# Kernel optimization log

Hardware: AMD Instinct MI355X
Metric: run time of the kernel (lower is better)

Reference implementation:

```python
import jax, jax.numpy as jnp
import numpy as np

N, E, G, H, IN = 200000, 400000, 64, 128, 5
LN_EPS = 1e-5


def setup_inputs() -> dict:
    key = jax.random.key(0)
    ks = jax.random.split(key, 32)
    d = {}
    d["x"] = jax.random.normal(ks[0], (N, IN), jnp.float32)
    d["edge_index"] = jax.random.randint(ks[1], (2, E), 0, N, dtype=jnp.int32)
    d["edge_attr"] = jax.random.normal(ks[2], (E, 1), jnp.float32)
    d["batch"] = jnp.sort(jax.random.randint(ks[3], (N,), 0, G, dtype=jnp.int32))
    dims = [IN, H, H]
    i = 4
    names = [("ew", "eb", "w1_", "b1_", "w2_", "b2_", "g", "bt")]
    for l, din in enumerate(dims):
        d[f"ew{l}"] = jax.random.normal(ks[i], (1, din), jnp.float32); i += 1
        d[f"eb{l}"] = jnp.zeros((din,), jnp.float32)
        d[f"w1_{l}"] = jax.random.normal(ks[i], (din, H), jnp.float32) / np.sqrt(din); i += 1
        d[f"b1_{l}"] = jnp.zeros((H,), jnp.float32)
        d[f"w2_{l}"] = jax.random.normal(ks[i], (H, H), jnp.float32) / np.sqrt(H); i += 1
        d[f"b2_{l}"] = jnp.zeros((H,), jnp.float32)
        d[f"g{l}"] = jnp.ones((H,), jnp.float32)
        d[f"bt{l}"] = jnp.zeros((H,), jnp.float32)
    return d


def _gine_layer(x, src, dst, edge_attr, ew, eb, w1, b1, w2, b2, g, bt):
    # edge encoder: Linear(1, din)
    e = edge_attr @ ew + eb                       # [E, din]
    # GINEConv message: ReLU(x_j + e), aggregated (sum) at destination
    m = jax.nn.relu(x[src] + e)                   # [E, din]
    aggr = jax.ops.segment_sum(m, dst, num_segments=N)  # [N, din]
    h = x + aggr                                  # (1 + eps)*x with eps=0
    # GIN MLP: Linear -> ReLU -> Linear
    h = jax.nn.relu(h @ w1 + b1) @ w2 + b2        # [N, H]
    # LayerNorm
    mu = jnp.mean(h, axis=-1, keepdims=True)
    var = jnp.mean((h - mu) ** 2, axis=-1, keepdims=True)
    h = (h - mu) * jax.lax.rsqrt(var + LN_EPS) * g + bt
    return jax.nn.relu(h)


def reference(x, edge_index, edge_attr, batch,
              ew0, eb0, w1_0, b1_0, w2_0, b2_0, g0, bt0,
              ew1, eb1, w1_1, b1_1, w2_1, b2_1, g1, bt1,
              ew2, eb2, w1_2, b1_2, w2_2, b2_2, g2, bt2):
    src, dst = edge_index[0], edge_index[1]
    x = _gine_layer(x, src, dst, edge_attr, ew0, eb0, w1_0, b1_0, w2_0, b2_0, g0, bt0)
    x = _gine_layer(x, src, dst, edge_attr, ew1, eb1, w1_1, b1_1, w2_1, b2_1, g1, bt1)
    x = _gine_layer(x, src, dst, edge_attr, ew2, eb2, w1_2, b1_2, w2_2, b2_2, g2, bt2)
    # global pooling per graph
    add_pool = jax.ops.segment_sum(x, batch, num_segments=G)           # [G, H]
    counts = jax.ops.segment_sum(jnp.ones((N,), x.dtype), batch, num_segments=G)
    mean_pool = add_pool / jnp.maximum(counts, 1.0)[:, None]           # [G, H]
    return jnp.concatenate([mean_pool, add_pool], axis=1)              # [G, 2H]
```

## Files before the change

### kernel.cpp

```cpp
#include <hip/hip_runtime.h>

#define N_NODES 200000
#define N_EDGES 400000
#define N_GRAPHS 64
#define HDIM 128
#define INDIM 5
#define LN_EPS 1e-5f
#define LDA 140
#define NPBLK 64

typedef __attribute__((ext_vector_type(8))) short short8;
typedef __attribute__((ext_vector_type(4))) float f32x4;
typedef __attribute__((ext_vector_type(2))) float f32x2;

__device__ __forceinline__ unsigned short to_bf(float v) {
    unsigned u = __builtin_bit_cast(unsigned, v);
    return (unsigned short)((u + 0x7FFFu + ((u >> 16) & 1u)) >> 16);
}
__device__ __forceinline__ float bf_lo(unsigned w) { return __builtin_bit_cast(float, w << 16); }
__device__ __forceinline__ float bf_hi(unsigned w) { return __builtin_bit_cast(float, w & 0xFFFF0000u); }
__device__ __forceinline__ float bf2f(unsigned short h) { return __builtin_bit_cast(float, (unsigned)h << 16); }

__device__ __forceinline__ unsigned short cvt1_bf(float v) {
    unsigned r;
    asm("v_cvt_pk_bf16_f32 %0, %1, %1" : "=v"(r) : "v"(v));
    return (unsigned short)r;
}
__device__ __forceinline__ unsigned cvt2_bf(float lo, float hi) {
    unsigned r;
    asm("v_cvt_pk_bf16_f32 %0, %1, %2" : "=v"(r) : "v"(lo), "v"(hi));
    return r;
}
__device__ __forceinline__ f32x2 vmax0(f32x2 v) {
#if __has_builtin(__builtin_elementwise_max)
    return __builtin_elementwise_max(v, (f32x2)0.f);
#else
    v.x = fmaxf(v.x, 0.f);
    v.y = fmaxf(v.y, 0.f);
    return v;
#endif
}

#define GLOAD(p0, p1, p2, p3, srcrow)                                       \
    {                                                                       \
        const uint4* xs_ = (const uint4*)(xin + (size_t)(srcrow)*128 + c0); \
        p0 = xs_[0]; p1 = xs_[1]; p2 = xs_[2]; p3 = xs_[3];                 \
    }

#define GP2(wd, i0)            \
    {                          \
        float4 wb_ = ep[i0];   \
        f32x2 xv_;             \
        xv_.x = bf_lo(wd);     \
        xv_.y = bf_hi(wd);     \
        f32x2 ew_, eb_;        \
        ew_.x = wb_.x;         \
        ew_.y = wb_.y;         \
        eb_.x = wb_.z;         \
        eb_.y = wb_.w;         \
        f32x2 t_ = xv_ + eb_;  \
        t_ = av2_ * ew_ + t_;  \
        accv[i0] += vmax0(t_); \
    }

#define GPROC(p0, p1, p2, p3, a_)                               \
    {                                                           \
        f32x2 av2_;                                             \
        av2_.x = (a_);                                          \
        av2_.y = (a_);                                          \
        GP2(p0.x, 0) GP2(p0.y, 1) GP2(p0.z, 2) GP2(p0.w, 3)     \
        GP2(p1.x, 4) GP2(p1.y, 5) GP2(p1.z, 6) GP2(p1.w, 7)     \
        GP2(p2.x, 8) GP2(p2.y, 9) GP2(p2.z, 10) GP2(p2.w, 11)   \
        GP2(p3.x, 12) GP2(p3.y, 13) GP2(p3.z, 14) GP2(p3.w, 15) \
    }

#define GI2(wd, i0)             \
    {                           \
        accv[i0].x = bf_lo(wd); \
        accv[i0].y = bf_hi(wd); \
    }

#define GINIT(p0, p1, p2, p3)                                   \
    {                                                           \
        GI2(p0.x, 0) GI2(p0.y, 1) GI2(p0.z, 2) GI2(p0.w, 3)     \
        GI2(p1.x, 4) GI2(p1.y, 5) GI2(p1.z, 6) GI2(p1.w, 7)     \
        GI2(p2.x, 8) GI2(p2.y, 9) GI2(p2.z, 10) GI2(p2.w, 11)   \
        GI2(p3.x, 12) GI2(p3.y, 13) GI2(p3.z, 14) GI2(p3.w, 15) \
    }


__global__ void hist_kernel(const int* __restrict__ ei, int* __restrict__ deg) {
    int e = blockIdx.x * blockDim.x + threadIdx.x;
    if (e < N_EDGES) atomicAdd(&deg[ei[N_EDGES + e]], 1);
}

__global__ void gbounds(const int* __restrict__ batch, int* __restrict__ gbnd) {
    int g = threadIdx.x;
    if (g > N_GRAPHS) return;
    int lo = 0, hi = N_NODES;
    while (lo < hi) {
        int mid = (lo + hi) >> 1;
        if (batch[mid] < g) lo = mid + 1;
        else hi = mid;
    }
    gbnd[g] = lo;
}

__global__ __launch_bounds__(256) void gsort(const int* __restrict__ deg,
                                             const int* __restrict__ gbnd,
                                             int* __restrict__ perm) {
    __shared__ int bins[64], offs[64];
    int g = blockIdx.x;
    int s = gbnd[g], e2 = gbnd[g + 1];
    int t = threadIdx.x;
    if (t < 64) bins[t] = 0;
    __syncthreads();
    for (int i = s + t; i < e2; i += 256) atomicAdd(&bins[min(deg[i], 63)], 1);
    __syncthreads();
    if (t == 0) {
        int run = 0;
        for (int b = 0; b < 64; ++b) { offs[b] = run; run += bins[b]; }
    }
    __syncthreads();
    if (t < 64) bins[t] = 0;
    __syncthreads();
    for (int i = s + t; i < e2; i += 256) {
        int b = min(deg[i], 63);
        int r = atomicAdd(&bins[b], 1);
        perm[s + offs[b] + r] = i;
    }
}

#define SCAN_CHUNK 1024
#define SCAN_BLOCKS ((N_NODES + SCAN_CHUNK - 1) / SCAN_CHUNK)

__global__ __launch_bounds__(256) void scan_phaseA(const int* __restrict__ deg, int* __restrict__ bsums,
                                                   int* __restrict__ poolz) {
    if (blockIdx.x == 0) {
        for (int i = threadIdx.x; i < N_GRAPHS * HDIM + N_GRAPHS; i += 256) poolz[i] = 0;
    }
    __shared__ int red[256];
    int t = threadIdx.x;
    int base = blockIdx.x * SCAN_CHUNK + t * 4;
    int s = 0;
#pragma unroll
    for (int k = 0; k < 4; ++k) {
        int i = base + k;
        s += (i < N_NODES) ? deg[i] : 0;
    }
    red[t] = s;
    __syncthreads();
    for (int off = 128; off; off >>= 1) {
        if (t < off) red[t] += red[t + off];
        __syncthreads();
    }
    if (t == 0) bsums[blockIdx.x] = red[0];
}

__global__ __launch_bounds__(256) void scan_phaseB(int* __restrict__ bsums, int* __restrict__ row_ptr) {
    __shared__ int s[256];
    int t = threadIdx.x;
    int v = (t < SCAN_BLOCKS) ? bsums[t] : 0;
    s[t] = v;
    __syncthreads();
    for (int off = 1; off < 256; off <<= 1) {
        int add = (t >= off) ? s[t - off] : 0;
        __syncthreads();
        s[t] += add;
        __syncthreads();
    }
    if (t < SCAN_BLOCKS) bsums[t] = s[t] - v;
    if (t == SCAN_BLOCKS - 1) row_ptr[N_NODES] = s[t];
}

__global__ __launch_bounds__(256) void scan_phaseC(const int* __restrict__ deg,
                                                   const int* __restrict__ bsums,
                                                   int* __restrict__ row_ptr,
                                                   int* __restrict__ cursor) {
    __shared__ int ts[256];
    int t = threadIdx.x;
    int base = blockIdx.x * SCAN_CHUNK + t * 4;
    int v[4];
    int s = 0;
#pragma unroll
    for (int k = 0; k < 4; ++k) {
        int i = base + k;
        v[k] = (i < N_NODES) ? deg[i] : 0;
        s += v[k];
    }
    ts[t] = s;
    __syncthreads();
    for (int off = 1; off < 256; off <<= 1) {
        int add = (t >= off) ? ts[t - off] : 0;
        __syncthreads();
        ts[t] += add;
        __syncthreads();
    }
    int run = bsums[blockIdx.x] + ts[t] - s;
#pragma unroll
    for (int k = 0; k < 4; ++k) {
        int i = base + k;
        if (i < N_NODES) { row_ptr[i] = run; cursor[i] = 0; }
        run += v[k];
    }
}

#define SCATTER_BLOCKS ((N_EDGES + 255) / 256)

__global__ void scatter_pack(const int* __restrict__ ei, const float* __restrict__ ea,
                             const int* __restrict__ row_ptr, int* __restrict__ cursor,
                             int2* __restrict__ csr,
                             const float* __restrict__ s0, short* __restrict__ d0,
                             const float* __restrict__ s1, short* __restrict__ d1,
                             const float* __restrict__ s2, short* __restrict__ d2,
                             const float* __restrict__ s3, short* __restrict__ d3,
                             const float* __restrict__ s4, short* __restrict__ d4,
                             const float* __restrict__ s5, short* __restrict__ d5) {
    int b = blockIdx.x;
    if (b < SCATTER_BLOCKS) {
        int e = b * 256 + threadIdx.x;
        if (e >= N_EDGES) return;
        int d = ei[N_EDGES + e];
        int pos = atomicAdd(&cursor[d], 1);
        csr[row_ptr[d] + pos] = make_int2(ei[e], __float_as_int(ea[e]));
        return;
    }
    b -= SCATTER_BLOCKS;
    const float* W;
    short* D;
    int din, KP, b0;
    if (b < 16)       { W = s0; D = d0; din = 5;   KP = 32;  b0 = 0; }
    else if (b < 80)  { W = s1; D = d1; din = 128; KP = 128; b0 = 16; }
    else if (b < 144) { W = s2; D = d2; din = 128; KP = 128; b0 = 80; }
    else if (b < 208) { W = s3; D = d3; din = 128; KP = 128; b0 = 144; }
    else if (b < 272) { W = s4; D = d4; din = 128; KP = 128; b0 = 208; }
    else              { W = s5; D = d5; din = 128; KP = 128; b0 = 272; }
    int idx = (b - b0) * 256 + threadIdx.x;
    if (idx >= KP * 128) return;
    int j = idx & 7;
    int lane = (idx >> 3) & 63;
    int rest = idx >> 9;
    int KS = KP >> 5;
    int kstep = rest % KS;
    int tile = rest / KS;
    int k = kstep * 32 + ((lane >> 4) * 8) + j;
    int n = tile * 16 + (lane & 15);
    float v = (k < din) ? W[k * 128 + n] : 0.f;
    D[idx] = (short)to_bf(v);
}

template <int KP1, bool POOL>
__global__ __launch_bounds__(256, 4) void layer_fused(
    const void* __restrict__ xin_v, const int* __restrict__ row_ptr,
    const int2* __restrict__ csr, const int* __restrict__ perm,
    const float* __restrict__ ew, const float* __restrict__ eb,
    const short* __restrict__ w1h, const float* __restrict__ b1,
    const short* __restrict__ w2h, const float* __restrict__ b2,
    const float* __restrict__ g, const float* __restrict__ bt,
    unsigned short* __restrict__ xout,
    const int* __restrict__ batch, float* __restrict__ pool, int* __restrict__ cnt) {
    __shared__ __align__(16) unsigned short A16[NPBLK * LDA];
    __shared__ int bidx[NPBLK];
    __shared__ int pidx[NPBLK];
    union Scratch {
        float4 eweb4[4 * 17];
        float part[KP1 == 128 ? 1 : NPBLK][4][INDIM];
    };
    __shared__ __align__(16) Scratch u;

    int tid = threadIdx.x;
    int node0 = blockIdx.x * NPBLK;

    if (tid >= 128 && tid < 192) pidx[tid - 128] = perm[node0 + tid - 128];

    if constexpr (KP1 == 128) {
        const unsigned short* xin = (const unsigned short*)xin_v;
        if (tid < 64) {
            int qq = tid >> 4, ii = tid & 15, c = qq * 32 + ii * 2;
            u.eweb4[qq * 17 + ii] = make_float4(ew[c], ew[c + 1], eb[c], eb[c + 1]);
        }
        if (POOL && tid >= 64 && tid < 128) bidx[tid - 64] = batch[perm[node0 + tid - 64]];

        int row = tid >> 2, qt = tid & 3, c0 = qt * 32;
        int prow = perm[node0 + row];

        const uint4* xn = (const uint4*)(xin + (size_t)prow * 128 + c0);
        uint4 o0 = xn[0], o1 = xn[1], o2 = xn[2], o3 = xn[3];
        int beg = row_ptr[prow], end = row_ptr[prow + 1];

        uint4 va0, va1, va2, va3;
        float aA = 0.f;
        int2 rC = make_int2(0, 0), rD = rC;
        if (beg < end) {
            int2 r = csr[beg];
            aA = __int_as_float(r.y);
            GLOAD(va0, va1, va2, va3, r.x);
        }
        if (beg + 1 < end) rC = csr[beg + 1];
        if (beg + 2 < end) rD = csr[beg + 2];
        __syncthreads();
        const float4* ep = u.eweb4 + qt * 17;

        f32x2 accv[16];
        GINIT(o0, o1, o2, o3);

        int e = beg;
        while (e + 1 < end) {
            GPROC(va0, va1, va2, va3, aA);
            aA = __int_as_float(rC.y);
            GLOAD(va0, va1, va2, va3, rC.x);
            rC = rD;
            int i3 = min(e + 3, end - 1);
            rD = csr[i3];
            ++e;
        }
        if (e < end) GPROC(va0, va1, va2, va3, aA);

        uint2* Ar2 = (uint2*)&A16[row * LDA + c0];
#pragma unroll
        for (int k = 0; k < 8; ++k) {
            Ar2[k] = make_uint2(cvt2_bf(accv[2 * k].x, accv[2 * k].y),
                                cvt2_bf(accv[2 * k + 1].x, accv[2 * k + 1].y));
        }
    } else {
        const float* xinf = (const float*)xin_v;
        int row = tid >> 2, qt = tid & 3;
        int prow = perm[node0 + row];
        {
            float w[INDIM], b[INDIM], acc[INDIM];
#pragma unroll
            for (int j = 0; j < INDIM; ++j) {
                w[j] = ew[j];
                b[j] = eb[j];
                acc[j] = 0.f;
            }
            int beg = row_ptr[prow], end = row_ptr[prow + 1];
            int2 r;
            if (beg + qt < end) r = csr[beg + qt];
            for (int e = beg + qt; e < end; e += 4) {
                int2 rn = (e + 4 < end) ? csr[e + 4] : r;
                float a = __int_as_float(r.y);
#pragma unroll
                for (int j = 0; j < INDIM; ++j)
                    acc[j] += fmaxf(fmaf(a, w[j], xinf[r.x * INDIM + j] + b[j]), 0.f);
                r = rn;
            }
#pragma unroll
            for (int j = 0; j < INDIM; ++j) u.part[row][qt][j] = acc[j];
        }
        __syncthreads();
        if (tid < NPBLK) {
#pragma unroll
            for (int j = 0; j < INDIM; ++j) {
                float v = xinf[pidx[tid] * INDIM + j] + u.part[tid][0][j] + u.part[tid][1][j] +
                          u.part[tid][2][j] + u.part[tid][3][j];
                A16[tid * LDA + j] = cvt1_bf(v);
            }
#pragma unroll
            for (int j = INDIM; j < 32; ++j) A16[tid * LDA + j] = 0;
        }
        __syncthreads();
    }

    int wv = tid >> 6, lane = tid & 63;
    int mrow = lane & 15, q = lane >> 4;
    int arow = wv * 16 + mrow;

    const short8* w1p = (const short8*)w1h;
    const short8* w2p = (const short8*)w2h;

    f32x4 acc2[8];
#pragma unroll
    for (int t = 0; t < 8; ++t) acc2[t] = (f32x4){0.f, 0.f, 0.f, 0.f};
    constexpr int KS1 = KP1 / 32;
#pragma unroll
    for (int ks = 0; ks < KS1; ++ks) {
        short8 bh[8];
#pragma unroll
        for (int t = 0; t < 8; ++t) bh[t] = w1p[((size_t)t * KS1 + ks) * 64 + lane];
        short8 ah = *(const short8*)&A16[arow * LDA + ks * 32 + q * 8];
#pragma unroll
        for (int t = 0; t < 8; ++t)
            acc2[t] = __builtin_amdgcn_mfma_f32_16x16x32_bf16(ah, bh[t], acc2[t], 0, 0, 0);
    }
    {
        float b1v[8];
#pragma unroll
        for (int t = 0; t < 8; ++t) b1v[t] = b1[t * 16 + mrow];
#pragma unroll
        for (int t = 0; t < 8; ++t)
#pragma unroll
            for (int r = 0; r < 4; ++r) {
                int rrow = wv * 16 + q * 4 + r;
                int col = t * 16 + mrow;
                A16[rrow * LDA + col] = cvt1_bf(fmaxf(acc2[t][r] + b1v[t], 0.f));
            }
    }

#pragma unroll
    for (int t = 0; t < 8; ++t) acc2[t] = (f32x4){0.f, 0.f, 0.f, 0.f};
#pragma unroll
    for (int ks = 0; ks < 4; ++ks) {
        short8 bh[8];
#pragma unroll
        for (int t = 0; t < 8; ++t) bh[t] = w2p[((size_t)t * 4 + ks) * 64 + lane];
        short8 ah = *(const short8*)&A16[arow * LDA + ks * 32 + q * 8];
#pragma unroll
        for (int t = 0; t < 8; ++t)
            acc2[t] = __builtin_amdgcn_mfma_f32_16x16x32_bf16(ah, bh[t], acc2[t], 0, 0, 0);
    }

    float s4[4] = {0.f, 0.f, 0.f, 0.f}, q4[4] = {0.f, 0.f, 0.f, 0.f};
    {
        float b2v[8];
#pragma unroll
        for (int t = 0; t < 8; ++t) b2v[t] = b2[t * 16 + mrow];
#pragma unroll
        for (int t = 0; t < 8; ++t)
#pragma unroll
            for (int r = 0; r < 4; ++r) {
                float v = acc2[t][r] + b2v[t];
                acc2[t][r] = v;
                s4[r] += v;
                q4[r] += v * v;
            }
    }
#pragma unroll
    for (int m = 1; m <= 8; m <<= 1) {
#pragma unroll
        for (int r = 0; r < 4; ++r) {
            s4[r] += __shfl_xor(s4[r], m, 64);
            q4[r] += __shfl_xor(q4[r], m, 64);
        }
    }
    float mu[4], inv[4];
#pragma unroll
    for (int r = 0; r < 4; ++r) {
        mu[r] = s4[r] * (1.f / HDIM);
        float var = q4[r] * (1.f / HDIM) - mu[r] * mu[r];
        inv[r] = rsqrtf(var + LN_EPS);
    }
    float gv[8], btv[8];
#pragma unroll
    for (int t = 0; t < 8; ++t) {
        gv[t] = g[t * 16 + mrow];
        btv[t] = bt[t * 16 + mrow];
    }

#pragma unroll
    for (int t = 0; t < 8; ++t)
#pragma unroll
        for (int r = 0; r < 4; ++r) {
            int rrow = wv * 16 + q * 4 + r;
            int col = t * 16 + mrow;
            float o = fmaxf((acc2[t][r] - mu[r]) * inv[r] * gv[t] + btv[t], 0.f);
            A16[rrow * LDA + col] = cvt1_bf(o);
        }
    __syncthreads();

    if (!POOL) {
        unsigned* xo = (unsigned*)xout;
#pragma unroll
        for (int i = 0; i < 16; ++i) {
            int idx = tid + 256 * i;
            int row = idx >> 6, w = idx & 63;
            xo[(size_t)pidx[row] * 64 + w] = ((const unsigned*)&A16[row * LDA])[w];
        }
    } else {
        if (tid < 128) {
            int col = tid;
            float accp = 0.f;
            int cur = bidx[0];
            for (int r = 0; r < NPBLK; ++r) {
                int gi = bidx[r];
                if (gi != cur) {
                    unsafeAtomicAdd(&pool[cur * HDIM + col], accp);
                    accp = 0.f;
                    cur = gi;
                }
                accp += bf2f(A16[r * LDA + col]);
            }
            unsafeAtomicAdd(&pool[cur * HDIM + col], accp);
        } else if (tid == 255) {
            int cur = bidx[0], c = 0;
            for (int r = 0; r < NPBLK; ++r) {
                if (bidx[r] != cur) {
                    atomicAdd(&cnt[cur], c);
                    c = 0;
                    cur = bidx[r];
                }
                ++c;
            }
            atomicAdd(&cnt[cur], c);
        }
    }
}

__global__ void pool_final(const float* __restrict__ pool, const int* __restrict__ cnt,
                           float* __restrict__ out) {
    int g = blockIdx.x, j = threadIdx.x;
    float add = pool[g * HDIM + j];
    float c = (float)max(cnt[g], 1);
    out[g * (2 * HDIM) + j] = add / c;
    out[g * (2 * HDIM) + HDIM + j] = add;
}

extern "C" void kernel_launch(void* const* d_in, const int* in_sizes, int n_in,
                              void* d_out, int out_size, void* d_ws, size_t ws_size,
                              hipStream_t stream) {
    const float* x_in = (const float*)d_in[0];
    const int* ei = (const int*)d_in[1];
    const float* ea = (const float*)d_in[2];
    const int* batch = (const int*)d_in[3];
    const float* P[24];
    for (int i = 0; i < 24; ++i) P[i] = (const float*)d_in[4 + i];

    unsigned short* x_a = (unsigned short*)d_ws;
    unsigned short* x_b = x_a + (size_t)N_NODES * HDIM;
    float* pool = (float*)(x_b + (size_t)N_NODES * HDIM);
    int* cnt = (int*)(pool + N_GRAPHS * HDIM);
    int* deg = cnt + N_GRAPHS;
    int* cursor = deg + N_NODES;
    int* row_ptr = cursor + N_NODES;
    int* bsums = row_ptr + N_NODES + 1;
    int* gbnd = bsums + 256;
    int* perm = gbnd + 128;
    int2* csr = (int2*)(((uintptr_t)(perm + N_NODES) + 15) & ~(uintptr_t)15);
    short* wp = (short*)(((uintptr_t)(csr + N_EDGES) + 15) & ~(uintptr_t)15);
    float* out = (float*)d_out;

    short *w1h[3], *w2h[3];
    for (int l = 0; l < 3; ++l) {
        w1h[l] = wp + (size_t)l * 32768;
        w2h[l] = w1h[l] + 16384;
    }

    hipMemsetAsync(deg, 0, N_NODES * sizeof(int), stream);

    hist_kernel<<<(N_EDGES + 255) / 256, 256, 0, stream>>>(ei, deg);
    gbounds<<<1, 128, 0, stream>>>(batch, gbnd);
    gsort<<<N_GRAPHS, 256, 0, stream>>>(deg, gbnd, perm);

    scan_phaseA<<<SCAN_BLOCKS, 256, 0, stream>>>(deg, bsums, (int*)pool);
    scan_phaseB<<<1, 256, 0, stream>>>(bsums, row_ptr);
    scan_phaseC<<<SCAN_BLOCKS, 256, 0, stream>>>(deg, bsums, row_ptr, cursor);

    scatter_pack<<<SCATTER_BLOCKS + 336, 256, 0, stream>>>(
        ei, ea, row_ptr, cursor, csr,
        P[2], w1h[0], P[4], w2h[0],
        P[10], w1h[1], P[12], w2h[1],
        P[18], w1h[2], P[20], w2h[2]);

    layer_fused<32, false><<<N_NODES / NPBLK, 256, 0, stream>>>(
        x_in, row_ptr, csr, perm, P[0], P[1],
        w1h[0], P[3], w2h[0], P[5], P[6], P[7], x_a, nullptr, nullptr, nullptr);
    layer_fused<128, false><<<N_NODES / NPBLK, 256, 0, stream>>>(
        x_a, row_ptr, csr, perm, P[8], P[9],
        w1h[1], P[11], w2h[1], P[13], P[14], P[15], x_b, nullptr, nullptr, nullptr);
    layer_fused<128, true><<<N_NODES / NPBLK, 256, 0, stream>>>(
        x_b, row_ptr, csr, perm, P[16], P[17],
        w1h[2], P[19], w2h[2], P[21], P[22], P[23], nullptr, batch, pool, cnt);

    pool_final<<<N_GRAPHS, HDIM, 0, stream>>>(pool, cnt, out);
}
```

Measured before the change: 344.5 us.

## Double-buffer neighbor gathers in fused GINE layer and pad LDS to cap occupancy

The CSR edge-gather loop now keeps two neighbor feature rows in flight (va/vb register sets) and prefetches four CSR entries ahead, processing two edges per iteration, to hide global load latency. The __syncthreads is moved after the accumulator init so the initial loads overlap with more work. A dummy 10KB LDS array, written only under a never-true condition, is added to reduce blocks per CU, presumably to limit cache contention or give headroom for the extra registers. The added registers and lower occupancy may hurt latency hiding elsewhere.

```diff
diff --git a/kernel.cpp b/kernel.cpp
--- a/kernel.cpp
+++ b/kernel.cpp
@@ -262,6 +262,7 @@
     __shared__ __align__(16) unsigned short A16[NPBLK * LDA];
     __shared__ int bidx[NPBLK];
     __shared__ int pidx[NPBLK];
+    __shared__ int lds_pad[2560];
     union Scratch {
         float4 eweb4[4 * 17];
         float part[KP1 == 128 ? 1 : NPBLK][4][INDIM];
@@ -270,6 +271,7 @@
 
     int tid = threadIdx.x;
     int node0 = blockIdx.x * NPBLK;
+    if (row_ptr[N_NODES] < 0) lds_pad[tid] = tid;
 
     if (tid >= 128 && tid < 192) pidx[tid - 128] = perm[node0 + tid - 128];
 
@@ -288,33 +290,50 @@
         uint4 o0 = xn[0], o1 = xn[1], o2 = xn[2], o3 = xn[3];
         int beg = row_ptr[prow], end = row_ptr[prow + 1];
 
-        uint4 va0, va1, va2, va3;
-        float aA = 0.f;
-        int2 rC = make_int2(0, 0), rD = rC;
+        uint4 va0, va1, va2, va3, vb0, vb1, vb2, vb3;
+        float aA = 0.f, aB = 0.f;
+        int2 rC = make_int2(0, 0), rD = rC, rE = rC, rF = rC;
         if (beg < end) {
             int2 r = csr[beg];
             aA = __int_as_float(r.y);
             GLOAD(va0, va1, va2, va3, r.x);
         }
-        if (beg + 1 < end) rC = csr[beg + 1];
-        if (beg + 2 < end) rD = csr[beg + 2];
-        __syncthreads();
-        const float4* ep = u.eweb4 + qt * 17;
-
+        if (beg + 1 < end) {
+            int2 r = csr[beg + 1];
+            aB = __int_as_float(r.y);
+            GLOAD(vb0, vb1, vb2, vb3, r.x);
+        }
+        if (beg + 2 < end) rC = csr[beg + 2];
+        if (beg + 3 < end) rD = csr[beg + 3];
+        if (beg < end) {
+            rE = csr[min(beg + 4, end - 1)];
+            rF = csr[min(beg + 5, end - 1)];
+        }
         f32x2 accv[16];
         GINIT(o0, o1, o2, o3);
+        __syncthreads();
+        const float4* ep = u.eweb4 + qt * 17;
 
         int e = beg;
-        while (e + 1 < end) {
+        while (e + 3 < end) {
             GPROC(va0, va1, va2, va3, aA);
             aA = __int_as_float(rC.y);
             GLOAD(va0, va1, va2, va3, rC.x);
-            rC = rD;
-            int i3 = min(e + 3, end - 1);
-            rD = csr[i3];
-            ++e;
+            GPROC(vb0, vb1, vb2, vb3, aB);
+            aB = __int_as_float(rD.y);
+            GLOAD(vb0, vb1, vb2, vb3, rD.x);
+            rC = rE;
+            rD = rF;
+            rE = csr[min(e + 6, end - 1)];
+            rF = csr[min(e + 7, end - 1)];
+            e += 2;
         }
         if (e < end) GPROC(va0, va1, va2, va3, aA);
+        if (e + 1 < end) GPROC(vb0, vb1, vb2, vb3, aB);
+        if (e + 2 < end) {
+            GLOAD(va0, va1, va2, va3, rC.x);
+            GPROC(va0, va1, va2, va3, __int_as_float(rC.y));
+        }
 
         uint2* Ar2 = (uint2*)&A16[row * LDA + c0];
 #pragma unroll
```

After: 408.5 us. 1.19x slower.

## Fold per-graph degree bucketing into the scan kernels, dropping gbounds and gsort

Applied to the files above, without the earlier changes.

Removes the separate gbounds and gsort kernels and folds the node permutation into the existing scan phases. Phase A builds a global (graph, degree bucket) histogram with 16 degree buckets, phase B scans it into cursors, and phase C scatters node ids into perm with atomics. This cuts two launches and the 64-block gsort, which has poor parallelism, at the cost of global atomics on 1024 bins. It also coarsens degree bucketing from 64 to 16 levels, and the order within a bucket becomes nondeterministic.

```diff
diff --git a/kernel.cpp b/kernel.cpp
--- a/kernel.cpp
+++ b/kernel.cpp
@@ -8,6 +8,8 @@
 #define LN_EPS 1e-5f
 #define LDA 140
 #define NPBLK 64
+#define NB 16
+#define NGB (N_GRAPHS * NB)
 
 typedef __attribute__((ext_vector_type(8))) short short8;
 typedef __attribute__((ext_vector_type(4))) float f32x4;
@@ -94,48 +96,13 @@
     if (e < N_EDGES) atomicAdd(&deg[ei[N_EDGES + e]], 1);
 }
 
-__global__ void gbounds(const int* __restrict__ batch, int* __restrict__ gbnd) {
-    int g = threadIdx.x;
-    if (g > N_GRAPHS) return;
-    int lo = 0, hi = N_NODES;
-    while (lo < hi) {
-        int mid = (lo + hi) >> 1;
-        if (batch[mid] < g) lo = mid + 1;
-        else hi = mid;
-    }
-    gbnd[g] = lo;
-}
-
-__global__ __launch_bounds__(256) void gsort(const int* __restrict__ deg,
-                                             const int* __restrict__ gbnd,
-                                             int* __restrict__ perm) {
-    __shared__ int bins[64], offs[64];
-    int g = blockIdx.x;
-    int s = gbnd[g], e2 = gbnd[g + 1];
-    int t = threadIdx.x;
-    if (t < 64) bins[t] = 0;
-    __syncthreads();
-    for (int i = s + t; i < e2; i += 256) atomicAdd(&bins[min(deg[i], 63)], 1);
-    __syncthreads();
-    if (t == 0) {
-        int run = 0;
-        for (int b = 0; b < 64; ++b) { offs[b] = run; run += bins[b]; }
-    }
-    __syncthreads();
-    if (t < 64) bins[t] = 0;
-    __syncthreads();
-    for (int i = s + t; i < e2; i += 256) {
-        int b = min(deg[i], 63);
-        int r = atomicAdd(&bins[b], 1);
-        perm[s + offs[b] + r] = i;
-    }
-}
-
 #define SCAN_CHUNK 1024
 #define SCAN_BLOCKS ((N_NODES + SCAN_CHUNK - 1) / SCAN_CHUNK)
 
 __global__ __launch_bounds__(256) void scan_phaseA(const int* __restrict__ deg, int* __restrict__ bsums,
-                                                   int* __restrict__ poolz) {
+                                                   int* __restrict__ poolz,
+                                                   const int* __restrict__ batch,
+                                                   int* __restrict__ gb_bins) {
     if (blockIdx.x == 0) {
         for (int i = threadIdx.x; i < N_GRAPHS * HDIM + N_GRAPHS; i += 256) poolz[i] = 0;
     }
@@ -146,7 +113,11 @@
 #pragma unroll
     for (int k = 0; k < 4; ++k) {
         int i = base + k;
-        s += (i < N_NODES) ? deg[i] : 0;
+        if (i < N_NODES) {
+            int d = deg[i];
+            s += d;
+            atomicAdd(&gb_bins[batch[i] * NB + min(d, NB - 1)], 1);
+        }
     }
     red[t] = s;
     __syncthreads();
@@ -157,7 +128,9 @@
     if (t == 0) bsums[blockIdx.x] = red[0];
 }
 
-__global__ __launch_bounds__(256) void scan_phaseB(int* __restrict__ bsums, int* __restrict__ row_ptr) {
+__global__ __launch_bounds__(256) void scan_phaseB(int* __restrict__ bsums, int* __restrict__ row_ptr,
+                                                   const int* __restrict__ gb_bins,
+                                                   int* __restrict__ gb_cur) {
     __shared__ int s[256];
     int t = threadIdx.x;
     int v = (t < SCAN_BLOCKS) ? bsums[t] : 0;
@@ -171,12 +144,32 @@
     }
     if (t < SCAN_BLOCKS) bsums[t] = s[t] - v;
     if (t == SCAN_BLOCKS - 1) row_ptr[N_NODES] = s[t];
+    __syncthreads();
+
+    int w0 = gb_bins[t * 4], w1 = gb_bins[t * 4 + 1], w2 = gb_bins[t * 4 + 2], w3 = gb_bins[t * 4 + 3];
+    int sum4 = w0 + w1 + w2 + w3;
+    s[t] = sum4;
+    __syncthreads();
+    for (int off = 1; off < 256; off <<= 1) {
+        int add = (t >= off) ? s[t - off] : 0;
+        __syncthreads();
+        s[t] += add;
+        __syncthreads();
+    }
+    int run = s[t] - sum4;
+    gb_cur[t * 4] = run;
+    gb_cur[t * 4 + 1] = run + w0;
+    gb_cur[t * 4 + 2] = run + w0 + w1;
+    gb_cur[t * 4 + 3] = run + w0 + w1 + w2;
 }
 
 __global__ __launch_bounds__(256) void scan_phaseC(const int* __restrict__ deg,
                                                    const int* __restrict__ bsums,
                                                    int* __restrict__ row_ptr,
-                                                   int* __restrict__ cursor) {
+                                                   int* __restrict__ cursor,
+                                                   const int* __restrict__ batch,
+                                                   int* __restrict__ gb_cur,
+                                                   int* __restrict__ perm) {
     __shared__ int ts[256];
     int t = threadIdx.x;
     int base = blockIdx.x * SCAN_CHUNK + t * 4;
@@ -200,7 +193,13 @@
 #pragma unroll
     for (int k = 0; k < 4; ++k) {
         int i = base + k;
-        if (i < N_NODES) { row_ptr[i] = run; cursor[i] = 0; }
+        if (i < N_NODES) {
+            row_ptr[i] = run;
+            cursor[i] = 0;
+            int idx = batch[i] * NB + min(v[k], NB - 1);
+            int pos = atomicAdd(&gb_cur[idx], 1);
+            perm[pos] = i;
+        }
         run += v[k];
     }
 }
@@ -520,11 +519,12 @@
     float* pool = (float*)(x_b + (size_t)N_NODES * HDIM);
     int* cnt = (int*)(pool + N_GRAPHS * HDIM);
     int* deg = cnt + N_GRAPHS;
-    int* cursor = deg + N_NODES;
+    int* gb_bins = deg + N_NODES;
+    int* gb_cur = gb_bins + NGB;
+    int* cursor = gb_cur + NGB;
     int* row_ptr = cursor + N_NODES;
     int* bsums = row_ptr + N_NODES + 1;
-    int* gbnd = bsums + 256;
-    int* perm = gbnd + 128;
+    int* perm = bsums + 256;
     int2* csr = (int2*)(((uintptr_t)(perm + N_NODES) + 15) & ~(uintptr_t)15);
     short* wp = (short*)(((uintptr_t)(csr + N_EDGES) + 15) & ~(uintptr_t)15);
     float* out = (float*)d_out;
@@ -535,15 +535,12 @@
         w2h[l] = w1h[l] + 16384;
     }
 
-    hipMemsetAsync(deg, 0, N_NODES * sizeof(int), stream);
+    hipMemsetAsync(deg, 0, (N_NODES + NGB) * sizeof(int), stream);
 
     hist_kernel<<<(N_EDGES + 255) / 256, 256, 0, stream>>>(ei, deg);
-    gbounds<<<1, 128, 0, stream>>>(batch, gbnd);
-    gsort<<<N_GRAPHS, 256, 0, stream>>>(deg, gbnd, perm);
-
-    scan_phaseA<<<SCAN_BLOCKS, 256, 0, stream>>>(deg, bsums, (int*)pool);
-    scan_phaseB<<<1, 256, 0, stream>>>(bsums, row_ptr);
-    scan_phaseC<<<SCAN_BLOCKS, 256, 0, stream>>>(deg, bsums, row_ptr, cursor);
+    scan_phaseA<<<SCAN_BLOCKS, 256, 0, stream>>>(deg, bsums, (int*)pool, batch, gb_bins);
+    scan_phaseB<<<1, 256, 0, stream>>>(bsums, row_ptr, gb_bins, gb_cur);
+    scan_phaseC<<<SCAN_BLOCKS, 256, 0, stream>>>(deg, bsums, row_ptr, cursor, batch, gb_cur, perm);
 
     scatter_pack<<<SCATTER_BLOCKS + 336, 256, 0, stream>>>(
         ei, ea, row_ptr, cursor, csr,
```

Result: slower. 389.1 us (+12.9%).
